# Kernel tuning notes

Measured on AMD Instinct MI355X. Metric: run time of the kernel, lower is better.

Reference implementation:

```python
import math
import jax, jax.numpy as jnp
import numpy as np

EPS = 1e-7  # K.epsilon()
ANCHORS = np.array([[10, 14], [23, 27], [37, 58], [81, 82], [135, 169], [344, 319]], np.float32)
ANCHOR_MASK = [[3, 4, 5], [0, 1, 2]]  # tiny-yolo, num_layers = 2
NUM_CLASSES = 80
IGNORE_THRESH = 0.5


def _decode(feats, anchors, input_shape):
    # feats: (B,H,W,3*(5+C)) -> raw_pred (B,H,W,3,5+C), pred_xy, pred_wh (normalized xywh)
    B, H, W, _ = feats.shape
    na = anchors.shape[0]
    feats = feats.reshape(B, H, W, na, 5 + NUM_CLASSES)
    gy, gx = jnp.meshgrid(jnp.arange(H, dtype=feats.dtype), jnp.arange(W, dtype=feats.dtype), indexing='ij')
    grid = jnp.stack([gx, gy], -1)[None, :, :, None, :]  # (1,H,W,1,2) in (x,y)
    box_xy = (jax.nn.sigmoid(feats[..., :2]) + grid) / jnp.array([W, H], feats.dtype)
    box_wh = jnp.exp(feats[..., 2:4]) * anchors[None, None, None, :, :] / input_shape[::-1]
    return feats, box_xy, box_wh


def _box_ciou(b_true, b_pred):
    # b_true: (B,T,4) xywh, b_pred: (B,H,W,A,4) xywh -> ciou, iou: (B,H,W,A,T)
    bt = b_true[:, None, None, None, :, :]   # (B,1,1,1,T,4)
    bp = b_pred[..., None, :]                # (B,H,W,A,1,4)
    t_xy, t_wh = bt[..., :2], bt[..., 2:4]
    p_xy, p_wh = bp[..., :2], bp[..., 2:4]
    t_min, t_max = t_xy - t_wh / 2.0, t_xy + t_wh / 2.0
    p_min, p_max = p_xy - p_wh / 2.0, p_xy + p_wh / 2.0
    i_wh = jnp.maximum(jnp.minimum(t_max, p_max) - jnp.maximum(t_min, p_min), 0.0)
    inter = i_wh[..., 0] * i_wh[..., 1]
    union = t_wh[..., 0] * t_wh[..., 1] + p_wh[..., 0] * p_wh[..., 1] - inter
    iou = inter / (union + EPS)
    center = jnp.sum(jnp.square(t_xy - p_xy), -1)
    e_wh = jnp.maximum(jnp.maximum(t_max, p_max) - jnp.minimum(t_min, p_min), 0.0)
    diag = jnp.sum(jnp.square(e_wh), -1)
    diou = iou - center / (diag + EPS)
    v = 4.0 * jnp.square(jnp.arctan2(t_wh[..., 0], t_wh[..., 1]) - jnp.arctan2(p_wh[..., 0], p_wh[..., 1])) / (math.pi * math.pi)
    alpha = jax.lax.stop_gradient(v / (1.0 - iou + v + EPS))
    return diou - alpha * v, iou


def _bce_logits(target, logits):
    # numerically stable sigmoid BCE with logits (matches K.binary_crossentropy from_logits=True)
    return jnp.maximum(logits, 0.0) - logits * target + jnp.log1p(jnp.exp(-jnp.abs(logits)))


def setup_inputs() -> dict:
    key = jax.random.key(0)
    ks = jax.random.split(key, 10)
    B, T = 64, 100
    output0 = jax.random.normal(ks[0], (B, 13, 13, 255), jnp.float32) * 0.5
    output1 = jax.random.normal(ks[1], (B, 26, 26, 255), jnp.float32) * 0.5
    xy = jax.random.uniform(ks[2], (B, T, 2), jnp.float32)
    wh = jax.random.uniform(ks[3], (B, T, 2), jnp.float32, minval=0.05, maxval=0.3)
    y_true_box = jnp.concatenate([xy, wh], -1)
    iou_mask0 = (jax.random.uniform(ks[4], (B, 13, 13, 3, T)) < 0.01).astype(jnp.float32)
    iou_mask1 = (jax.random.uniform(ks[5], (B, 26, 26, 3, T)) < 0.01).astype(jnp.float32)
    class0 = jax.nn.one_hot(jax.random.randint(ks[6], (B, 13, 13, 3), 0, NUM_CLASSES), NUM_CLASSES) * (jax.random.uniform(ks[7], (B, 13, 13, 3, 1)) < 0.7)
    class1 = jax.nn.one_hot(jax.random.randint(ks[8], (B, 26, 26, 3), 0, NUM_CLASSES), NUM_CLASSES) * (jax.random.uniform(ks[9], (B, 26, 26, 3, 1)) < 0.7)
    return {"output0": output0, "output1": output1, "y_true_box": y_true_box,
            "iou_mask0": iou_mask0, "iou_mask1": iou_mask1, "class0": class0, "class1": class1}


def reference(output0, output1, y_true_box, iou_mask0, iou_mask1, class0, class1):
    outputs = [output0, output1]
    masks = [iou_mask0, iou_mask1]
    classes = [class0, class1]
    input_shape = jnp.asarray(output0.shape[1:3], jnp.float32) * 32.0  # (h,w)
    batch_f = jnp.float32(output0.shape[0])
    loss = total_loc = total_conf = total_cls = jnp.float32(0.0)
    for i in range(2):
        anchors = jnp.asarray(ANCHORS[ANCHOR_MASK[i]])
        raw_pred, pred_xy, pred_wh = _decode(outputs[i], anchors, input_shape)
        pred_box = jnp.concatenate([pred_xy, pred_wh], -1)  # (B,H,W,3,4)
        ciou, iou = _box_ciou(y_true_box, pred_box)         # (B,H,W,3,T)
        best_iou = jnp.max(iou, -1)                         # (B,H,W,3)
        ignore = (best_iou < IGNORE_THRESH)[..., None]
        ignore_match = (best_iou > IGNORE_THRESH)[..., None]
        class_id_match = jax.lax.stop_gradient(
            (jnp.max(jax.nn.sigmoid(raw_pred[..., 5:]), -1) < 0.25)[..., None] & ignore_match)
        ignore_mask = (ignore | class_id_match).astype(jnp.float32)
        ciou_loss = jnp.sum((1.0 - ciou) * masks[i], -1, keepdims=True)  # (B,H,W,3,1)
        obj = jnp.max(masks[i], -1, keepdims=True)  # true_objectness_probs
        bce_obj = _bce_logits(obj, raw_pred[..., 4:5])
        confidence_loss = obj * bce_obj + (1.0 - obj) * bce_obj * ignore_mask
        class_loss = obj * _bce_logits(classes[i], raw_pred[..., 5:])
        class_sum = jnp.sum(classes[i], -1, keepdims=True)
        class_sum = class_sum + (class_sum == 0).astype(jnp.float32)
        location_loss = jnp.sum(ciou_loss / class_sum) / batch_f
        confidence_loss = jnp.sum(confidence_loss) / batch_f
        class_loss = jnp.sum(class_loss) / batch_f
        loss = loss + location_loss + confidence_loss + class_loss
        total_loc = total_loc + location_loss
        total_conf = total_conf + confidence_loss
        total_cls = total_cls + class_loss
    return loss, total_loc, total_conf, total_cls
```

## Files before the change

kernel.cpp:

```cpp
#include <hip/hip_runtime.h>
#include <math.h>

#define T_BOX 100
#define NCLS 80
constexpr float EPSF = 1e-7f;
constexpr float INV416 = 1.0f / 416.0f;
constexpr float LOGIT25 = -1.0986122886681098f;

__device__ __forceinline__ float rcpf_(float x) { return __builtin_amdgcn_rcpf(x); }
__device__ __forceinline__ float sigmoidf_(float x) { return rcpf_(1.0f + __expf(-x)); }
__device__ __forceinline__ float softplus_abs_(float x) {
    return __logf(1.0f + __expf(-fabsf(x)));
}

__device__ __forceinline__ float atan2_pos_(float y, float x) {
    const float mn = fminf(y, x), mx = fmaxf(y, x);
    const float r  = mn * rcpf_(mx);
    const float r2 = r * r;
    float p = fmaf(r2, 0.0208351f, -0.0851330f);
    p = fmaf(r2, p, 0.1801410f);
    p = fmaf(r2, p, -0.3302995f);
    p = fmaf(r2, p, 0.9998660f);
    const float a = r * p;
    return (y > x) ? (1.5707963268f - a) : a;
}

__constant__ float c_anc[2][3][2] = {
    {{81.0f, 82.0f}, {135.0f, 169.0f}, {344.0f, 319.0f}},
    {{10.0f, 14.0f}, {23.0f, 27.0f}, {37.0f, 58.0f}},
};

#define CELLS0 507
#define CELLS1 2028
#define CELLS_TOT 2535
#define GRP_PER_BLK 16
#define BLK_PER_BATCH 159

__device__ __forceinline__ float red16_add(float v) {
    v += __shfl_xor(v, 1); v += __shfl_xor(v, 2);
    v += __shfl_xor(v, 4); v += __shfl_xor(v, 8);
    return v;
}
__device__ __forceinline__ float red16_max(float v) {
    v = fmaxf(v, __shfl_xor(v, 1)); v = fmaxf(v, __shfl_xor(v, 2));
    v = fmaxf(v, __shfl_xor(v, 4)); v = fmaxf(v, __shfl_xor(v, 8));
    return v;
}

__global__ __launch_bounds__(256) void yolo_fused_kernel(
    const float* __restrict__ pred0, const float* __restrict__ mask0, const float* __restrict__ cls0,
    const float* __restrict__ pred1, const float* __restrict__ mask1, const float* __restrict__ cls1,
    const float* __restrict__ ytrue,
    float* __restrict__ ws, int nshard)
{
    __shared__ float s_tx[T_BOX], s_ty[T_BOX], s_nx[T_BOX], s_ny[T_BOX],
                     s_xx[T_BOX], s_xy[T_BOX], s_ar[T_BOX], s_at[T_BOX];
    __shared__ float s_acc[6];

    const int b = blockIdx.y;
    const int tid = threadIdx.x;

    if (tid < T_BOX) {
        const float4 yt = *reinterpret_cast<const float4*>(ytrue + ((size_t)b * T_BOX + tid) * 4);
        s_tx[tid] = yt.x; s_ty[tid] = yt.y;
        s_nx[tid] = yt.x - 0.5f * yt.z; s_ny[tid] = yt.y - 0.5f * yt.w;
        s_xx[tid] = yt.x + 0.5f * yt.z; s_xy[tid] = yt.y + 0.5f * yt.w;
        s_ar[tid] = yt.z * yt.w; s_at[tid] = atan2_pos_(yt.z, yt.w);
    }
    if (tid < 6) s_acc[tid] = 0.0f;
    __syncthreads();

    const int l   = tid & 15;
    const int grp = tid >> 4;
    const int r   = (int)blockIdx.x * GRP_PER_BLK + grp;

    if (r < CELLS_TOT) {
        int level, W, H, cell, ncell;
        const float *pred, *mask, *cls;
        float invWH;
        if (r < CELLS0) {
            level = 0; W = 13; H = 13; cell = r; ncell = CELLS0;
            invWH = 1.0f / 13.0f;
            pred = pred0; mask = mask0; cls = cls0;
        } else {
            level = 1; W = 26; H = 26; cell = r - CELLS0; ncell = CELLS1;
            invWH = 1.0f / 26.0f;
            pred = pred1; mask = mask1; cls = cls1;
        }

        const int a  = cell % 3;
        const int hw = cell / 3;
        const int w  = hw % W;
        const int h  = hw / W;

        const float* p = pred + ((size_t)((b * H + h) * W + w)) * 255 + a * 85;

        const float aw = c_anc[level][a][0];
        const float ah = c_anc[level][a][1];

        const float px = (sigmoidf_(p[0]) + (float)w) * invWH;
        const float py = (sigmoidf_(p[1]) + (float)h) * invWH;
        const float pw = __expf(p[2]) * aw * INV416;
        const float ph = __expf(p[3]) * ah * INV416;

        const float pminx = px - 0.5f * pw, pminy = py - 0.5f * ph;
        const float pmaxx = px + 0.5f * pw, pmaxy = py + 0.5f * ph;
        const float parea = pw * ph;
        const float patan = atan2_pos_(pw, ph);
        const float c4pi2 = 4.0f / (float)(M_PI * M_PI);

        const float* m = mask + ((size_t)b * ncell + cell) * (size_t)T_BOX;

        float maxd = -1e30f, obj = 0.0f, locsum = 0.0f;

        float mv_[7];
        #pragma unroll
        for (int k = 0; k < 6; ++k) mv_[k] = m[l + 16 * k];
        mv_[6] = (l < 4) ? m[l + 96] : 0.0f;

        auto body = [&](int t, float mv) {
            const float nx = s_nx[t], ny = s_ny[t], xx = s_xx[t], xy = s_xy[t];
            const float iwx = fmaxf(fminf(xx, pmaxx) - fmaxf(nx, pminx), 0.0f);
            const float iwy = fmaxf(fminf(xy, pmaxy) - fmaxf(ny, pminy), 0.0f);
            const float inter = iwx * iwy;
            const float sa = s_ar[t] + parea;
            maxd = fmaxf(maxd, fmaf(3.0f, inter, -sa));
            obj  = fmaxf(obj, mv);
            if (mv != 0.0f) {
                const float uni = sa - inter;
                const float iou = inter * rcpf_(uni + EPSF);
                const float dx = s_tx[t] - px, dy = s_ty[t] - py;
                const float center = dx * dx + dy * dy;
                const float ewx = fmaxf(fmaxf(xx, pmaxx) - fminf(nx, pminx), 0.0f);
                const float ewy = fmaxf(fmaxf(xy, pmaxy) - fminf(ny, pminy), 0.0f);
                const float diag = ewx * ewx + ewy * ewy;
                const float diou = iou - center * rcpf_(diag + EPSF);
                const float dv = s_at[t] - patan;
                const float v = c4pi2 * dv * dv;
                const float alpha = v * rcpf_(1.0f - iou + v + EPSF);
                const float ciou = diou - alpha * v;
                locsum += (1.0f - ciou) * mv;
            }
        };

        #pragma unroll
        for (int k = 0; k < 6; ++k) body(l + 16 * k, mv_[k]);
        if (l < 4) body(l + 96, mv_[6]);

        obj  = red16_max(obj);
        maxd = red16_max(maxd);

        const float x4 = p[4];
        const float bce = fmaxf(x4, 0.0f) - x4 * obj + softplus_abs_(x4);

        float loc = 0.0f, conf, clsl = 0.0f;

        if (obj > 0.0f) {
            const float* cp = cls + ((size_t)b * ncell + cell) * (size_t)NCLS;
            float csum = 0.0f, bsum = 0.0f;
            #pragma unroll
            for (int k = 0; k < 5; ++k) {
                const int c = l + 16 * k;
                const float z = cp[c];
                const float x = p[5 + c];
                csum += z;
                bsum += fmaxf(x, 0.0f) - x * z + softplus_abs_(x);
            }
            locsum = red16_add(locsum);
            csum   = red16_add(csum);
            bsum   = red16_add(bsum);
            const float csum2 = csum + ((csum == 0.0f) ? 1.0f : 0.0f);
            loc  = locsum * rcpf_(csum2);
            clsl = bsum;
            conf = bce;
        } else {
            float ign;
            if (maxd > EPSF) {
                float maxlogit = -1e30f;
                #pragma unroll
                for (int k = 0; k < 5; ++k) maxlogit = fmaxf(maxlogit, p[5 + l + 16 * k]);
                maxlogit = red16_max(maxlogit);
                ign = (maxlogit < LOGIT25) ? 1.0f : 0.0f;
            } else {
                ign = (maxd < EPSF) ? 1.0f : 0.0f;
            }
            conf = bce * ign;
        }

        if (l == 0) {
            const int base = level * 3;
            atomicAdd(&s_acc[base + 0], loc);
            atomicAdd(&s_acc[base + 1], conf);
            atomicAdd(&s_acc[base + 2], clsl);
        }
    }

    __syncthreads();
    if (tid < 6) {
        const int shard = (int)((blockIdx.y * gridDim.x + blockIdx.x) % (unsigned)nshard);
        atomicAdd(&ws[shard * 16 + tid], s_acc[tid]);
    }
}

__global__ void yolo_finalize(const float* __restrict__ ws,
                              float* __restrict__ out, float invB, int nshard) {
    __shared__ float s_sum[6];
    const int t = threadIdx.x;
    if (t < 6) {
        float s = 0.0f;
        for (int i = 0; i < nshard; ++i) s += ws[i * 16 + t];
        s_sum[t] = s;
    }
    __syncthreads();
    if (t == 0) {
        const float loc  = (s_sum[0] + s_sum[3]) * invB;
        const float conf = (s_sum[1] + s_sum[4]) * invB;
        const float cls  = (s_sum[2] + s_sum[5]) * invB;
        out[0] = loc + conf + cls;
        out[1] = loc;
        out[2] = conf;
        out[3] = cls;
    }
}

extern "C" void kernel_launch(void* const* d_in, const int* in_sizes, int n_in,
                              void* d_out, int out_size, void* d_ws, size_t ws_size,
                              hipStream_t stream) {
    const float* out0  = (const float*)d_in[0];
    const float* out1  = (const float*)d_in[1];
    const float* ytrue = (const float*)d_in[2];
    const float* m0    = (const float*)d_in[3];
    const float* m1    = (const float*)d_in[4];
    const float* c0    = (const float*)d_in[5];
    const float* c1    = (const float*)d_in[6];
    float* out = (float*)d_out;
    float* ws  = (float*)d_ws;

    const int B = in_sizes[0] / (13 * 13 * 255);

    int nshard = (int)(ws_size / 64);
    if (nshard < 1)  nshard = 1;
    if (nshard > 64) nshard = 64;
    const size_t zero_bytes = (nshard == 1) ? 24 : (size_t)nshard * 64;

    hipMemsetAsync(ws, 0, zero_bytes, stream);

    dim3 grid(BLK_PER_BATCH, B);
    yolo_fused_kernel<<<grid, 256, 0, stream>>>(
        out0, m0, c0, out1, m1, c1, ytrue, ws, nshard);

    yolo_finalize<<<1, 64, 0, stream>>>(ws, out, 1.0f / (float)B, nshard);
}
```

Baseline: 51.51 us.

## Process four cell chunks per block and pack truth boxes into float4 LDS

```diff
diff --git a/kernel.cpp b/kernel.cpp
--- a/kernel.cpp
+++ b/kernel.cpp
@@ -34,7 +34,9 @@
 #define CELLS1 2028
 #define CELLS_TOT 2535
 #define GRP_PER_BLK 16
-#define BLK_PER_BATCH 159
+#define NCHUNK 4
+#define CELLS_PER_BLK 64
+#define BLK_PER_BATCH 40
 
 __device__ __forceinline__ float red16_add(float v) {
     v += __shfl_xor(v, 1); v += __shfl_xor(v, 2);
@@ -53,8 +55,8 @@
     const float* __restrict__ ytrue,
     float* __restrict__ ws, int nshard)
 {
-    __shared__ float s_tx[T_BOX], s_ty[T_BOX], s_nx[T_BOX], s_ny[T_BOX],
-                     s_xx[T_BOX], s_xy[T_BOX], s_ar[T_BOX], s_at[T_BOX];
+    __shared__ float4 s_box[T_BOX];
+    __shared__ float4 s_aux[T_BOX];
     __shared__ float s_acc[6];
 
     const int b = blockIdx.y;
@@ -62,19 +64,22 @@
 
     if (tid < T_BOX) {
         const float4 yt = *reinterpret_cast<const float4*>(ytrue + ((size_t)b * T_BOX + tid) * 4);
-        s_tx[tid] = yt.x; s_ty[tid] = yt.y;
-        s_nx[tid] = yt.x - 0.5f * yt.z; s_ny[tid] = yt.y - 0.5f * yt.w;
-        s_xx[tid] = yt.x + 0.5f * yt.z; s_xy[tid] = yt.y + 0.5f * yt.w;
-        s_ar[tid] = yt.z * yt.w; s_at[tid] = atan2_pos_(yt.z, yt.w);
+        s_box[tid] = make_float4(yt.x - 0.5f * yt.z, yt.y - 0.5f * yt.w,
+                                 yt.x + 0.5f * yt.z, yt.y + 0.5f * yt.w);
+        s_aux[tid] = make_float4(yt.x, yt.y, yt.z * yt.w, atan2_pos_(yt.z, yt.w));
     }
     if (tid < 6) s_acc[tid] = 0.0f;
     __syncthreads();
 
     const int l   = tid & 15;
     const int grp = tid >> 4;
-    const int r   = (int)blockIdx.x * GRP_PER_BLK + grp;
-
-    if (r < CELLS_TOT) {
+    const float c4pi2 = 4.0f / (float)(M_PI * M_PI);
+
+    #pragma unroll 1
+    for (int chunk = 0; chunk < NCHUNK; ++chunk) {
+        const int r = (int)blockIdx.x * CELLS_PER_BLK + chunk * GRP_PER_BLK + grp;
+        if (r >= CELLS_TOT) break;
+
         int level, W, H, cell, ncell;
         const float *pred, *mask, *cls;
         float invWH;
@@ -107,7 +112,6 @@
         const float pmaxx = px + 0.5f * pw, pmaxy = py + 0.5f * ph;
         const float parea = pw * ph;
         const float patan = atan2_pos_(pw, ph);
-        const float c4pi2 = 4.0f / (float)(M_PI * M_PI);
 
         const float* m = mask + ((size_t)b * ncell + cell) * (size_t)T_BOX;
 
@@ -119,23 +123,24 @@
         mv_[6] = (l < 4) ? m[l + 96] : 0.0f;
 
         auto body = [&](int t, float mv) {
-            const float nx = s_nx[t], ny = s_ny[t], xx = s_xx[t], xy = s_xy[t];
-            const float iwx = fmaxf(fminf(xx, pmaxx) - fmaxf(nx, pminx), 0.0f);
-            const float iwy = fmaxf(fminf(xy, pmaxy) - fmaxf(ny, pminy), 0.0f);
+            const float4 bx = s_box[t];
+            const float4 ax = s_aux[t];
+            const float iwx = fmaxf(fminf(bx.z, pmaxx) - fmaxf(bx.x, pminx), 0.0f);
+            const float iwy = fmaxf(fminf(bx.w, pmaxy) - fmaxf(bx.y, pminy), 0.0f);
             const float inter = iwx * iwy;
-            const float sa = s_ar[t] + parea;
+            const float sa = ax.z + parea;
             maxd = fmaxf(maxd, fmaf(3.0f, inter, -sa));
             obj  = fmaxf(obj, mv);
             if (mv != 0.0f) {
                 const float uni = sa - inter;
                 const float iou = inter * rcpf_(uni + EPSF);
-                const float dx = s_tx[t] - px, dy = s_ty[t] - py;
+                const float dx = ax.x - px, dy = ax.y - py;
                 const float center = dx * dx + dy * dy;
-                const float ewx = fmaxf(fmaxf(xx, pmaxx) - fminf(nx, pminx), 0.0f);
-                const float ewy = fmaxf(fmaxf(xy, pmaxy) - fminf(ny, pminy), 0.0f);
+                const float ewx = fmaxf(fmaxf(bx.z, pmaxx) - fminf(bx.x, pminx), 0.0f);
+                const float ewy = fmaxf(fmaxf(bx.w, pmaxy) - fminf(bx.y, pminy), 0.0f);
                 const float diag = ewx * ewx + ewy * ewy;
                 const float diou = iou - center * rcpf_(diag + EPSF);
-                const float dv = s_at[t] - patan;
+                const float dv = ax.w - patan;
                 const float v = c4pi2 * dv * dv;
                 const float alpha = v * rcpf_(1.0f - iou + v + EPSF);
                 const float ciou = diou - alpha * v;
```

After: 54.01 us. +4.9%, slower.
